# Kernel optimization log

Measured on AMD Instinct MI355X. Metric: run time of the kernel, lower is better.

Reference implementation:

```python
import jax, jax.numpy as jnp
import numpy as np

V = 16384      # total nodes
G = 32         # nodes per graph (512 graphs)
D = 256        # node embedding dim == hidden_size
N = 8          # heads
H = 32         # head size
I = 1024       # intermediate size
LN_EPS = 1e-12


def _layer_norm(x, g, b):
    mu = jnp.mean(x, axis=-1, keepdims=True)
    var = jnp.mean(jnp.square(x - mu), axis=-1, keepdims=True)
    return (x - mu) * jax.lax.rsqrt(var + LN_EPS) * g + b


def setup_inputs() -> dict:
    key = jax.random.key(0)
    ks = jax.random.split(key, 5)
    node_embeddings = jax.random.normal(ks[0], (V, D), jnp.float32)
    # fully-connected pairs within each graph of size G (sorted by source node)
    idx = np.arange(V, dtype=np.int32).reshape(-1, G)          # [num_graphs, G]
    src = np.repeat(idx, G, axis=1).reshape(-1)                # [P]
    dst = np.tile(idx, (1, G)).reshape(-1)                     # [P]
    in_graph_node_pairs = jnp.asarray(np.stack([src, dst], axis=-1))  # [P, 2]
    s = 0.02
    return {
        "node_embeddings": node_embeddings,
        "in_graph_node_pairs": in_graph_node_pairs,
        "W_qkv": jax.random.normal(ks[1], (D, 3 * N * H), jnp.float32) * s,
        "W_o": jax.random.normal(ks[2], (N * H, D), jnp.float32) * s,
        "ln1_g": jnp.ones((D,), jnp.float32),
        "ln1_b": jnp.zeros((D,), jnp.float32),
        "W_i": jax.random.normal(ks[3], (D, I), jnp.float32) * s,
        "W_out2": jax.random.normal(ks[4], (I, D), jnp.float32) * s,
        "ln2_g": jnp.ones((D,), jnp.float32),
        "ln2_b": jnp.zeros((D,), jnp.float32),
    }


def reference(node_embeddings, in_graph_node_pairs, W_qkv, W_o, ln1_g, ln1_b,
              W_i, W_out2, ln2_g, ln2_b):
    nV = node_embeddings.shape[0]
    src = in_graph_node_pairs[:, 0]
    dst = in_graph_node_pairs[:, 1]
    # QKV projection -> [V, N, 3H] -> split
    qkv = (node_embeddings @ W_qkv).reshape(nV, N, 3 * H)
    q, k, v = jnp.split(qkv, 3, axis=-1)                       # each [V, N, H]
    # per-pair scores [P, N]
    scores = jnp.einsum('phi,phi->ph', q[src], k[dst]) / jnp.sqrt(jnp.float32(H))
    # segment softmax over source node, all heads at once
    m = jax.ops.segment_max(scores, src, num_segments=nV)       # [V, N]
    e = jnp.exp(scores - m[src])
    denom = jax.ops.segment_sum(e, src, num_segments=nV)        # [V, N]
    w = e / denom[src]                                          # [P, N]
    # weighted value scatter-sum -> [V, N, H]
    wv = w[:, :, None] * v[dst]
    att = jax.ops.segment_sum(wv, src, num_segments=nV).reshape(nV, N * H)
    # output projection + residual + LN
    pre = _layer_norm(att @ W_o + node_embeddings, ln1_g, ln1_b)
    inter = jax.nn.gelu(pre @ W_i, approximate=False)
    out = _layer_norm(inter @ W_out2 + pre, ln2_g, ln2_b)
    return out
```

## Files before the change

### kernel.cpp

```cpp
#include <hip/hip_runtime.h>
#include <math.h>

#define V 16384
#define D 256
#define NH 256
#define THREE_NH 768
#define IDIM 1024
#define LN_EPS 1e-12f

typedef short s16x8 __attribute__((ext_vector_type(8)));
typedef float f32x4 __attribute__((ext_vector_type(4)));

__device__ inline unsigned short f2bf(float f) {
    unsigned u = __float_as_uint(f);
    u += 0x7fffu + ((u >> 16) & 1u);
    return (unsigned short)(u >> 16);
}
__device__ inline float bf2f(unsigned short s) {
    return __uint_as_float(((unsigned)s) << 16);
}
__device__ inline float bflo(unsigned v) { return __uint_as_float(v << 16); }
__device__ inline float bfhi(unsigned v) { return __uint_as_float(v & 0xffff0000u); }

__device__ inline void gl2lds16(const unsigned short* g, unsigned short* l) {
    __builtin_amdgcn_global_load_lds(
        (__attribute__((address_space(1))) void*)(g),
        (__attribute__((address_space(3))) void*)(l), 16, 0, 0);
}

template <int ROWS_T>
__device__ inline void stage(const unsigned short* __restrict__ src, size_t row0,
                             int ldk, int k0, unsigned short* lds, int wv, int lane) {
    constexpr int PER_WAVE = ROWS_T / 32;
    #pragma unroll
    for (int i = 0; i < PER_WAVE; ++i) {
        const int seg = wv * PER_WAVE + i;
        const int r = seg * 8 + (lane >> 3);
        const int c = (lane & 7) ^ (r & 7);
        gl2lds16(src + (row0 + (size_t)r) * ldk + k0 + c * 8, lds + seg * 512);
    }
}

__device__ inline s16x8 fragld(const unsigned short* lds, int row, int chunk) {
    return *(const s16x8*)&lds[row * 64 + ((chunk ^ (row & 7)) << 3)];
}

__global__ __launch_bounds__(256) void prep(const float* __restrict__ X,
                                            unsigned short* __restrict__ Xb,
                                            const float* __restrict__ Wqkv,
                                            const float* __restrict__ Wo,
                                            const float* __restrict__ Wi,
                                            const float* __restrict__ Wo2,
                                            unsigned short* __restrict__ WqkvT,
                                            unsigned short* __restrict__ WoT,
                                            unsigned short* __restrict__ WiT,
                                            unsigned short* __restrict__ Wo2T) {
    const int b = blockIdx.x, t = threadIdx.x;
    if (b >= 768) {
        int i = (b - 768) * 256 + t;
        float4 v = ((const float4*)X)[i];
        ushort4 o;
        o.x = f2bf(v.x); o.y = f2bf(v.y); o.z = f2bf(v.z); o.w = f2bf(v.w);
        ((ushort4*)Xb)[i] = o;
        return;
    }
    __shared__ float tile[32][33];
    const float* W; unsigned short* Wt; int K, N, bx, by;
    if (b < 192)      { W = Wqkv; Wt = WqkvT; K = 256;  N = 768;  bx = b & 7;          by = b >> 3; }
    else if (b < 256) { W = Wo;   Wt = WoT;   K = 256;  N = 256;  bx = (b - 192) & 7;  by = (b - 192) >> 3; }
    else if (b < 512) { W = Wi;   Wt = WiT;   K = 256;  N = 1024; bx = (b - 256) & 7;  by = (b - 256) >> 3; }
    else              { W = Wo2;  Wt = Wo2T;  K = 1024; N = 256;  bx = (b - 512) & 31; by = (b - 512) >> 5; }
    const int k0 = bx * 32, n0 = by * 32;
    #pragma unroll
    for (int p = 0; p < 4; ++p) {
        int idx = t + p * 256, r = idx >> 5, c = idx & 31;
        tile[r][c] = W[(size_t)(k0 + r) * N + n0 + c];
    }
    __syncthreads();
    #pragma unroll
    for (int p = 0; p < 4; ++p) {
        int idx = t + p * 256, r = idx >> 5, c = idx & 31;
        Wt[(size_t)(n0 + r) * K + k0 + c] = f2bf(tile[c][r]);
    }
}

template <int K, int N, int EPI>
__global__ __launch_bounds__(256) void gemm128(const unsigned short* __restrict__ A,
                                               const unsigned short* __restrict__ Bt,
                                               unsigned short* __restrict__ C) {
    __shared__ unsigned short As[128 * 64];
    __shared__ unsigned short Bs[128 * 64];
    constexpr int NCOL = N / 128;
    const int b = blockIdx.x;
    const int idx = b >> 3;
    const int r0 = ((b & 7) * 16 + idx / NCOL) * 128;
    const int c0 = (idx % NCOL) * 128;
    const int t = threadIdx.x;
    const int wv = t >> 6, lane = t & 63, q = lane >> 4, l16 = lane & 15;
    const int wr = (wv >> 1) * 64, wc = (wv & 1) * 64;
    f32x4 acc[4][4] = {};

    for (int k0 = 0; k0 < K; k0 += 64) {
        __syncthreads();
        stage<128>(A,  (size_t)r0, K, k0, As, wv, lane);
        stage<128>(Bt, (size_t)c0, K, k0, Bs, wv, lane);
        __builtin_amdgcn_s_waitcnt(0);
        __syncthreads();
        #pragma unroll
        for (int kk2 = 0; kk2 < 2; ++kk2) {
            s16x8 af[4], bfr[4];
            #pragma unroll
            for (int mf = 0; mf < 4; ++mf)
                af[mf] = fragld(As, wr + mf * 16 + l16, kk2 * 4 + q);
            #pragma unroll
            for (int nf = 0; nf < 4; ++nf)
                bfr[nf] = fragld(Bs, wc + nf * 16 + l16, kk2 * 4 + q);
            #pragma unroll
            for (int mf = 0; mf < 4; ++mf)
                #pragma unroll
                for (int nf = 0; nf < 4; ++nf)
                    acc[mf][nf] = __builtin_amdgcn_mfma_f32_16x16x32_bf16(af[mf], bfr[nf], acc[mf][nf], 0, 0, 0);
        }
    }

    #pragma unroll
    for (int mf = 0; mf < 4; ++mf)
        #pragma unroll
        for (int nf = 0; nf < 4; ++nf) {
            const int cg = c0 + wc + nf * 16 + l16;
            #pragma unroll
            for (int r = 0; r < 4; ++r) {
                const int rg = r0 + wr + mf * 16 + q * 4 + r;
                float v = acc[mf][nf][r];
                if (EPI == 1) v = 0.5f * v * (1.f + erff(v * 0.70710678118654752f));
                C[(size_t)rg * N + cg] = f2bf(v);
            }
        }
}

template <int K, bool OUTF, bool RESBF>
__global__ __launch_bounds__(256) void gemm_ln(const unsigned short* __restrict__ A,
                                               const unsigned short* __restrict__ Bt,
                                               const void* __restrict__ resv,
                                               const float* __restrict__ gamma,
                                               const float* __restrict__ beta,
                                               float* __restrict__ outf,
                                               unsigned short* __restrict__ outb) {
    __shared__ unsigned short As[2][32 * 64];
    __shared__ unsigned short Bs[2][256 * 64];
    __shared__ float2 partial[4][32];
    __shared__ float2 stats[32];
    const int t = threadIdx.x, r0 = blockIdx.x * 32;
    const int wv = t >> 6, lane = t & 63, q = lane >> 4, l16 = lane & 15;
    const int wc = wv * 64;
    f32x4 acc[2][4] = {};

    for (int k0 = 0; k0 < K; k0 += 128) {
        __syncthreads();
        stage<32>(A, (size_t)r0, K, k0,      As[0], wv, lane);
        stage<32>(A, (size_t)r0, K, k0 + 64, As[1], wv, lane);
        stage<256>(Bt, 0, K, k0,      Bs[0], wv, lane);
        stage<256>(Bt, 0, K, k0 + 64, Bs[1], wv, lane);
        __builtin_amdgcn_s_waitcnt(0);
        __syncthreads();
        #pragma unroll
        for (int sub = 0; sub < 2; ++sub) {
            #pragma unroll
            for (int kk2 = 0; kk2 < 2; ++kk2) {
                s16x8 af[2], bfr[4];
                #pragma unroll
                for (int mf = 0; mf < 2; ++mf)
                    af[mf] = fragld(As[sub], mf * 16 + l16, kk2 * 4 + q);
                #pragma unroll
                for (int nf = 0; nf < 4; ++nf)
                    bfr[nf] = fragld(Bs[sub], wc + nf * 16 + l16, kk2 * 4 + q);
                #pragma unroll
                for (int mf = 0; mf < 2; ++mf)
                    #pragma unroll
                    for (int nf = 0; nf < 4; ++nf)
                        acc[mf][nf] = __builtin_amdgcn_mfma_f32_16x16x32_bf16(af[mf], bfr[nf], acc[mf][nf], 0, 0, 0);
            }
        }
    }

    #pragma unroll
    for (int mf = 0; mf < 2; ++mf)
        #pragma unroll
        for (int nf = 0; nf < 4; ++nf) {
            const int cg = wc + nf * 16 + l16;
            #pragma unroll
            for (int r = 0; r < 4; ++r) {
                const size_t idx = (size_t)(r0 + mf * 16 + q * 4 + r) * NH + cg;
                float rv;
                if (RESBF) rv = bf2f(((const unsigned short*)resv)[idx]);
                else       rv = ((const float*)resv)[idx];
                acc[mf][nf][r] += rv;
            }
        }

    #pragma unroll
    for (int mf = 0; mf < 2; ++mf) {
        float s[4] = {0.f, 0.f, 0.f, 0.f}, ss[4] = {0.f, 0.f, 0.f, 0.f};
        #pragma unroll
        for (int nf = 0; nf < 4; ++nf)
            #pragma unroll
            for (int r = 0; r < 4; ++r) {
                float v = acc[mf][nf][r];
                s[r] += v; ss[r] += v * v;
            }
        #pragma unroll
        for (int off = 1; off < 16; off <<= 1)
            #pragma unroll
            for (int r = 0; r < 4; ++r) {
                s[r]  += __shfl_xor(s[r],  off);
                ss[r] += __shfl_xor(ss[r], off);
            }
        if (l16 == 0)
            #pragma unroll
            for (int r = 0; r < 4; ++r)
                partial[wv][mf * 16 + q * 4 + r] = make_float2(s[r], ss[r]);
    }
    __syncthreads();
    if (t < 32) {
        float s = 0.f, ss = 0.f;
        #pragma unroll
        for (int w = 0; w < 4; ++w) { s += partial[w][t].x; ss += partial[w][t].y; }
        float mu  = s * (1.f / 256.f);
        float var = ss * (1.f / 256.f) - mu * mu;
        stats[t] = make_float2(mu, rsqrtf(var + LN_EPS));
    }
    __syncthreads();

    #pragma unroll
    for (int mf = 0; mf < 2; ++mf)
        #pragma unroll
        for (int nf = 0; nf < 4; ++nf) {
            const int cg = wc + nf * 16 + l16;
            const float g = gamma[cg], b = beta[cg];
            #pragma unroll
            for (int r = 0; r < 4; ++r) {
                const int rl = mf * 16 + q * 4 + r;
                const float2 st = stats[rl];
                float v = (acc[mf][nf][r] - st.x) * st.y * g + b;
                const size_t idx = (size_t)(r0 + rl) * NH + cg;
                if (OUTF) outf[idx] = v;
                else      outb[idx] = f2bf(v);
            }
        }
}

#define LDR 776
__global__ __launch_bounds__(256) void attln(const unsigned short* __restrict__ qkv,
                                             const unsigned short* __restrict__ WoT,
                                             const float* __restrict__ X,
                                             const float* __restrict__ gamma,
                                             const float* __restrict__ beta,
                                             unsigned short* __restrict__ preb) {
    __shared__ unsigned short smem[33536 + 320];
    unsigned short* s  = smem;
    unsigned short* pt = smem + 24832;
    unsigned short* at = smem;
    unsigned short* Bs = smem + 8192;
    float2* partial = (float2*)(smem + 24832);
    float2* stats   = (float2*)(smem + 24832 + 512);

    const int g = blockIdx.x;
    const int t = threadIdx.x;
    const int h = t >> 5, u = t & 31;
    const int ub = u & 7;
    const int us = u >> 3;
    const int qc = h * 96;

    const unsigned short* src = qkv + (size_t)g * 32 * THREE_NH;
    #pragma unroll
    for (int pp = 0; pp < 12; ++pp) {
        int c = t + pp * 256;
        int row = c / 96, col8 = c % 96;
        s16x8 vv = *(const s16x8*)&src[c * 8];
        *(s16x8*)&s[row * LDR + col8 * 8] = vv;
    }
    __syncthreads();

    float sc[4][8];
    #pragma unroll
    for (int di = 0; di < 4; ++di)
        #pragma unroll
        for (int dj = 0; dj < 8; ++dj) sc[di][dj] = 0.f;

    for (int kq = 0; kq < 8; ++kq) {
        float qv[4][4];
        #pragma unroll
        for (int di = 0; di < 4; ++di) {
            uint2 v = *(const uint2*)&s[(ub + 8 * di) * LDR + qc + 4 * kq];
            qv[di][0] = bflo(v.x); qv[di][1] = bfhi(v.x);
            qv[di][2] = bflo(v.y); qv[di][3] = bfhi(v.y);
        }
        #pragma unroll
        for (int dj = 0; dj < 8; ++dj) {
            uint2 v = *(const uint2*)&s[(us + 4 * dj) * LDR + qc + 32 + 4 * kq];
            float kv[4];
            kv[0] = bflo(v.x); kv[1] = bfhi(v.x);
            kv[2] = bflo(v.y); kv[3] = bfhi(v.y);
            #pragma unroll
            for (int di = 0; di < 4; ++di)
                #pragma unroll
                for (int kk = 0; kk < 4; ++kk)
                    sc[di][dj] = fmaf(qv[di][kk], kv[kk], sc[di][dj]);
        }
    }

    #pragma unroll
    for (int di = 0; di < 4; ++di) {
        float m = sc[di][0];
        #pragma unroll
        for (int dj = 1; dj < 8; ++dj) m = fmaxf(m, sc[di][dj]);
        m = fmaxf(m, __shfl_xor(m, 8));
        m = fmaxf(m, __shfl_xor(m, 16));
        float sum = 0.f;
        #pragma unroll
        for (int dj = 0; dj < 8; ++dj) {
            float e = __expf((sc[di][dj] - m) * 0.17677669529663687f);
            sc[di][dj] = e;
            sum += e;
        }
        sum += __shfl_xor(sum, 8);
        sum += __shfl_xor(sum, 16);
        float inv = 1.f / sum;
        const int rb = h * 1088 + (ub + 8 * di) * 34;
        #pragma unroll
        for (int dj = 0; dj < 8; ++dj)
            pt[rb + us + 4 * dj] = f2bf(sc[di][dj] * inv);
    }
    __syncthreads();

    const int vc = qc + 64, d0 = us * 8;
    float o[4][8];
    #pragma unroll
    for (int di = 0; di < 4; ++di)
        #pragma unroll
        for (int dd = 0; dd < 8; ++dd) o[di][dd] = 0.f;

    for (int j = 0; j < 32; ++j) {
        float pv[4];
        #pragma unroll
        for (int di = 0; di < 4; ++di)
            pv[di] = bf2f(pt[h * 1088 + (ub + 8 * di) * 34 + j]);
        #pragma unroll
        for (int dq = 0; dq < 2; ++dq) {
            uint2 v = *(const uint2*)&s[j * LDR + vc + d0 + 4 * dq];
            float v0 = bflo(v.x), v1 = bfhi(v.x), v2 = bflo(v.y), v3 = bfhi(v.y);
            #pragma unroll
            for (int di = 0; di < 4; ++di) {
                o[di][dq * 4 + 0] = fmaf(pv[di], v0, o[di][dq * 4 + 0]);
                o[di][dq * 4 + 1] = fmaf(pv[di], v1, o[di][dq * 4 + 1]);
                o[di][dq * 4 + 2] = fmaf(pv[di], v2, o[di][dq * 4 + 2]);
                o[di][dq * 4 + 3] = fmaf(pv[di], v3, o[di][dq * 4 + 3]);
            }
        }
    }
    __syncthreads();

    {
        const int col = h * 32 + d0;
        const int kb = col >> 6, c = (col & 63) >> 3;
        #pragma unroll
        for (int di = 0; di < 4; ++di) {
            const int i = ub + 8 * di;
            s16x8 ov;
            #pragma unroll
            for (int dd = 0; dd < 8; ++dd) ov[dd] = (short)f2bf(o[di][dd]);
            *(s16x8*)&at[kb * 2048 + i * 64 + ((c ^ (i & 7)) << 3)] = ov;
        }
    }

    const int wv = t >> 6, lane = t & 63, q = lane >> 4, l16 = lane & 15;
    const int wc = wv * 64;
    const int r0 = g * 32;
    f32x4 acc[2][4] = {};

    for (int k0 = 0; k0 < 256; k0 += 64) {
        __syncthreads();
        stage<256>(WoT, 0, 256, k0, Bs, wv, lane);
        __builtin_amdgcn_s_waitcnt(0);
        __syncthreads();
        const unsigned short* atk = at + (k0 >> 6) * 2048;
        #pragma unroll
        for (int kk2 = 0; kk2 < 2; ++kk2) {
            s16x8 af[2], bfr[4];
            #pragma unroll
            for (int mf = 0; mf < 2; ++mf)
                af[mf] = fragld(atk, mf * 16 + l16, kk2 * 4 + q);
            #pragma unroll
            for (int nf = 0; nf < 4; ++nf)
                bfr[nf] = fragld(Bs, wc + nf * 16 + l16, kk2 * 4 + q);
            #pragma unroll
            for (int mf = 0; mf < 2; ++mf)
                #pragma unroll
                for (int nf = 0; nf < 4; ++nf)
                    acc[mf][nf] = __builtin_amdgcn_mfma_f32_16x16x32_bf16(af[mf], bfr[nf], acc[mf][nf], 0, 0, 0);
        }
    }

    #pragma unroll
    for (int mf = 0; mf < 2; ++mf)
        #pragma unroll
        for (int nf = 0; nf < 4; ++nf) {
            const int cg = wc + nf * 16 + l16;
            #pragma unroll
            for (int r = 0; r < 4; ++r)
                acc[mf][nf][r] += X[(size_t)(r0 + mf * 16 + q * 4 + r) * NH + cg];
        }

    #pragma unroll
    for (int mf = 0; mf < 2; ++mf) {
        float sp[4] = {0.f, 0.f, 0.f, 0.f}, ssp[4] = {0.f, 0.f, 0.f, 0.f};
        #pragma unroll
        for (int nf = 0; nf < 4; ++nf)
            #pragma unroll
            for (int r = 0; r < 4; ++r) {
                float v = acc[mf][nf][r];
                sp[r] += v; ssp[r] += v * v;
            }
        #pragma unroll
        for (int off = 1; off < 16; off <<= 1)
            #pragma unroll
            for (int r = 0; r < 4; ++r) {
                sp[r]  += __shfl_xor(sp[r],  off);
                ssp[r] += __shfl_xor(ssp[r], off);
            }
        if (l16 == 0)
            #pragma unroll
            for (int r = 0; r < 4; ++r)
                partial[wv * 32 + mf * 16 + q * 4 + r] = make_float2(sp[r], ssp[r]);
    }
    __syncthreads();
    if (t < 32) {
        float sv = 0.f, ssv = 0.f;
        #pragma unroll
        for (int w = 0; w < 4; ++w) { sv += partial[w * 32 + t].x; ssv += partial[w * 32 + t].y; }
        float mu  = sv * (1.f / 256.f);
        float var = ssv * (1.f / 256.f) - mu * mu;
        stats[t] = make_float2(mu, rsqrtf(var + LN_EPS));
    }
    __syncthreads();

    #pragma unroll
    for (int mf = 0; mf < 2; ++mf)
        #pragma unroll
        for (int nf = 0; nf < 4; ++nf) {
            const int cg = wc + nf * 16 + l16;
            const float gm = gamma[cg], bt = beta[cg];
            #pragma unroll
            for (int r = 0; r < 4; ++r) {
                const int rl = mf * 16 + q * 4 + r;
                const float2 st = stats[rl];
                float v = (acc[mf][nf][r] - st.x) * st.y * gm + bt;
                preb[(size_t)(r0 + rl) * NH + cg] = f2bf(v);
            }
        }
}

extern "C" void kernel_launch(void* const* d_in, const int* in_sizes, int n_in,
                              void* d_out, int out_size, void* d_ws, size_t ws_size,
                              hipStream_t stream) {
    const float* X      = (const float*)d_in[0];
    const float* W_qkv  = (const float*)d_in[2];
    const float* W_o    = (const float*)d_in[3];
    const float* ln1_g  = (const float*)d_in[4];
    const float* ln1_b  = (const float*)d_in[5];
    const float* W_i    = (const float*)d_in[6];
    const float* W_out2 = (const float*)d_in[7];
    const float* ln2_g  = (const float*)d_in[8];
    const float* ln2_b  = (const float*)d_in[9];
    float* out = (float*)d_out;

    char* ws = (char*)d_ws;
    unsigned short* Xbf   = (unsigned short*)(ws);
    unsigned short* qkvb  = (unsigned short*)(ws + 8388608);
    unsigned short* preb  = (unsigned short*)(ws + 58720256);
    unsigned short* WqkvT = (unsigned short*)(ws + 67108864);
    unsigned short* WoT   = (unsigned short*)(ws + 67502080);
    unsigned short* WiT   = (unsigned short*)(ws + 67633152);
    unsigned short* Wo2T  = (unsigned short*)(ws + 68157440);
    unsigned short* interb = (unsigned short*)(ws);

    dim3 blk(256);
    hipLaunchKernelGGL(prep, dim3(768 + V * D / 4 / 256), blk, 0, stream,
                       X, Xbf, W_qkv, W_o, W_i, W_out2, WqkvT, WoT, WiT, Wo2T);

    hipLaunchKernelGGL((gemm128<D, THREE_NH, 0>), dim3(V / 128 * (THREE_NH / 128)), blk, 0, stream,
                       Xbf, WqkvT, qkvb);
    hipLaunchKernelGGL(attln, dim3(V / 32), blk, 0, stream,
                       qkvb, WoT, X, ln1_g, ln1_b, preb);
    hipLaunchKernelGGL((gemm128<D, IDIM, 1>), dim3(V / 128 * (IDIM / 128)), blk, 0, stream,
                       preb, WiT, interb);
    hipLaunchKernelGGL((gemm_ln<IDIM, true, true>), dim3(V / 32), blk, 0, stream,
                       interb, Wo2T, (const void*)preb, ln2_g, ln2_b, out, (unsigned short*)nullptr);
}
```

Measured before the change: 158.5 us.

## Load GEMM fragments directly from global memory, drop LDS staging, use fast erf

All GEMM kernels (QKV, intermediate, output+LN, and the Wo projection inside the attention kernel) now load MFMA operand fragments straight from global memory into registers. This removes the LDS staging through global_load_lds and its per-k-step barriers. The GELU epilogue also replaces erff with a polynomial erf approximation using __expf. The cost is redundant global/L2 traffic, since waves no longer share tiles through LDS and the 16-byte row-strided loads are poorly coalesced. The erf approximation (about 1e-7 error) also slightly changes numerics.

```diff
diff --git a/kernel.cpp b/kernel.cpp
--- a/kernel.cpp
+++ b/kernel.cpp
@@ -22,23 +22,13 @@
 __device__ inline float bflo(unsigned v) { return __uint_as_float(v << 16); }
 __device__ inline float bfhi(unsigned v) { return __uint_as_float(v & 0xffff0000u); }
 
-__device__ inline void gl2lds16(const unsigned short* g, unsigned short* l) {
-    __builtin_amdgcn_global_load_lds(
-        (__attribute__((address_space(1))) void*)(g),
-        (__attribute__((address_space(3))) void*)(l), 16, 0, 0);
-}
-
-template <int ROWS_T>
-__device__ inline void stage(const unsigned short* __restrict__ src, size_t row0,
-                             int ldk, int k0, unsigned short* lds, int wv, int lane) {
-    constexpr int PER_WAVE = ROWS_T / 32;
-    #pragma unroll
-    for (int i = 0; i < PER_WAVE; ++i) {
-        const int seg = wv * PER_WAVE + i;
-        const int r = seg * 8 + (lane >> 3);
-        const int c = (lane & 7) ^ (r & 7);
-        gl2lds16(src + (row0 + (size_t)r) * ldk + k0 + c * 8, lds + seg * 512);
-    }
+__device__ inline float fast_erf(float x) {
+    float ax = fabsf(x);
+    float t  = 1.f / fmaf(0.3275911f, ax, 1.f);
+    float p  = fmaf(fmaf(fmaf(fmaf(1.061405429f, t, -1.453152027f), t,
+                              1.421413741f), t, -0.284496736f), t, 0.254829592f);
+    float e  = 1.f - p * t * __expf(-ax * ax);
+    return copysignf(e, x);
 }
 
 __device__ inline s16x8 fragld(const unsigned short* lds, int row, int chunk) {
@@ -85,11 +75,9 @@
 }
 
 template <int K, int N, int EPI>
-__global__ __launch_bounds__(256) void gemm128(const unsigned short* __restrict__ A,
-                                               const unsigned short* __restrict__ Bt,
-                                               unsigned short* __restrict__ C) {
-    __shared__ unsigned short As[128 * 64];
-    __shared__ unsigned short Bs[128 * 64];
+__global__ __launch_bounds__(256) void gemm_direct(const unsigned short* __restrict__ A,
+                                                   const unsigned short* __restrict__ Bt,
+                                                   unsigned short* __restrict__ C) {
     constexpr int NCOL = N / 128;
     const int b = blockIdx.x;
     const int idx = b >> 3;
@@ -100,27 +88,29 @@
     const int wr = (wv >> 1) * 64, wc = (wv & 1) * 64;
     f32x4 acc[4][4] = {};
 
+    const unsigned short* Ap = A  + (size_t)(r0 + wr + l16) * K;
+    const unsigned short* Bp = Bt + (size_t)(c0 + wc + l16) * K;
+
+    #pragma unroll
     for (int k0 = 0; k0 < K; k0 += 64) {
-        __syncthreads();
-        stage<128>(A,  (size_t)r0, K, k0, As, wv, lane);
-        stage<128>(Bt, (size_t)c0, K, k0, Bs, wv, lane);
-        __builtin_amdgcn_s_waitcnt(0);
-        __syncthreads();
-        #pragma unroll
-        for (int kk2 = 0; kk2 < 2; ++kk2) {
-            s16x8 af[4], bfr[4];
-            #pragma unroll
-            for (int mf = 0; mf < 4; ++mf)
-                af[mf] = fragld(As, wr + mf * 16 + l16, kk2 * 4 + q);
-            #pragma unroll
-            for (int nf = 0; nf < 4; ++nf)
-                bfr[nf] = fragld(Bs, wc + nf * 16 + l16, kk2 * 4 + q);
+        s16x8 af[4][2], bfr[4][2];
+        #pragma unroll
+        for (int mf = 0; mf < 4; ++mf)
+            #pragma unroll
+            for (int kk2 = 0; kk2 < 2; ++kk2)
+                af[mf][kk2] = *(const s16x8*)&Ap[(size_t)mf * 16 * K + k0 + (kk2 * 4 + q) * 8];
+        #pragma unroll
+        for (int nf = 0; nf < 4; ++nf)
+            #pragma unroll
+            for (int kk2 = 0; kk2 < 2; ++kk2)
+                bfr[nf][kk2] = *(const s16x8*)&Bp[(size_t)nf * 16 * K + k0 + (kk2 * 4 + q) * 8];
+        #pragma unroll
+        for (int kk2 = 0; kk2 < 2; ++kk2)
             #pragma unroll
             for (int mf = 0; mf < 4; ++mf)
                 #pragma unroll
                 for (int nf = 0; nf < 4; ++nf)
-                    acc[mf][nf] = __builtin_amdgcn_mfma_f32_16x16x32_bf16(af[mf], bfr[nf], acc[mf][nf], 0, 0, 0);
-        }
+                    acc[mf][nf] = __builtin_amdgcn_mfma_f32_16x16x32_bf16(af[mf][kk2], bfr[nf][kk2], acc[mf][nf], 0, 0, 0);
     }
 
     #pragma unroll
@@ -132,22 +122,20 @@
             for (int r = 0; r < 4; ++r) {
                 const int rg = r0 + wr + mf * 16 + q * 4 + r;
                 float v = acc[mf][nf][r];
-                if (EPI == 1) v = 0.5f * v * (1.f + erff(v * 0.70710678118654752f));
+                if (EPI == 1) v = 0.5f * v * (1.f + fast_erf(v * 0.70710678118654752f));
                 C[(size_t)rg * N + cg] = f2bf(v);
             }
         }
 }
 
 template <int K, bool OUTF, bool RESBF>
-__global__ __launch_bounds__(256) void gemm_ln(const unsigned short* __restrict__ A,
-                                               const unsigned short* __restrict__ Bt,
-                                               const void* __restrict__ resv,
-                                               const float* __restrict__ gamma,
-                                               const float* __restrict__ beta,
-                                               float* __restrict__ outf,
-                                               unsigned short* __restrict__ outb) {
-    __shared__ unsigned short As[2][32 * 64];
-    __shared__ unsigned short Bs[2][256 * 64];
+__global__ __launch_bounds__(256) void gemm_ln_direct(const unsigned short* __restrict__ A,
+                                                      const unsigned short* __restrict__ Bt,
+                                                      const void* __restrict__ resv,
+                                                      const float* __restrict__ gamma,
+                                                      const float* __restrict__ beta,
+                                                      float* __restrict__ outf,
+                                                      unsigned short* __restrict__ outb) {
     __shared__ float2 partial[4][32];
     __shared__ float2 stats[32];
     const int t = threadIdx.x, r0 = blockIdx.x * 32;
@@ -155,32 +143,29 @@
     const int wc = wv * 64;
     f32x4 acc[2][4] = {};
 
-    for (int k0 = 0; k0 < K; k0 += 128) {
-        __syncthreads();
-        stage<32>(A, (size_t)r0, K, k0,      As[0], wv, lane);
-        stage<32>(A, (size_t)r0, K, k0 + 64, As[1], wv, lane);
-        stage<256>(Bt, 0, K, k0,      Bs[0], wv, lane);
-        stage<256>(Bt, 0, K, k0 + 64, Bs[1], wv, lane);
-        __builtin_amdgcn_s_waitcnt(0);
-        __syncthreads();
-        #pragma unroll
-        for (int sub = 0; sub < 2; ++sub) {
-            #pragma unroll
-            for (int kk2 = 0; kk2 < 2; ++kk2) {
-                s16x8 af[2], bfr[4];
-                #pragma unroll
-                for (int mf = 0; mf < 2; ++mf)
-                    af[mf] = fragld(As[sub], mf * 16 + l16, kk2 * 4 + q);
+    const unsigned short* Ap = A  + (size_t)(r0 + l16) * K;
+    const unsigned short* Bp = Bt + (size_t)(wc + l16) * K;
+
+    #pragma unroll
+    for (int k0 = 0; k0 < K; k0 += 64) {
+        s16x8 af[2][2], bfr[4][2];
+        #pragma unroll
+        for (int mf = 0; mf < 2; ++mf)
+            #pragma unroll
+            for (int kk2 = 0; kk2 < 2; ++kk2)
+                af[mf][kk2] = *(const s16x8*)&Ap[(size_t)mf * 16 * K + k0 + (kk2 * 4 + q) * 8];
+        #pragma unroll
+        for (int nf = 0; nf < 4; ++nf)
+            #pragma unroll
+            for (int kk2 = 0; kk2 < 2; ++kk2)
+                bfr[nf][kk2] = *(const s16x8*)&Bp[(size_t)nf * 16 * K + k0 + (kk2 * 4 + q) * 8];
+        #pragma unroll
+        for (int kk2 = 0; kk2 < 2; ++kk2)
+            #pragma unroll
+            for (int mf = 0; mf < 2; ++mf)
                 #pragma unroll
                 for (int nf = 0; nf < 4; ++nf)
-                    bfr[nf] = fragld(Bs[sub], wc + nf * 16 + l16, kk2 * 4 + q);
-                #pragma unroll
-                for (int mf = 0; mf < 2; ++mf)
-                    #pragma unroll
-                    for (int nf = 0; nf < 4; ++nf)
-                        acc[mf][nf] = __builtin_amdgcn_mfma_f32_16x16x32_bf16(af[mf], bfr[nf], acc[mf][nf], 0, 0, 0);
-            }
-        }
+                    acc[mf][nf] = __builtin_amdgcn_mfma_f32_16x16x32_bf16(af[mf][kk2], bfr[nf][kk2], acc[mf][nf], 0, 0, 0);
     }
 
     #pragma unroll
@@ -260,7 +245,6 @@
     unsigned short* s  = smem;
     unsigned short* pt = smem + 24832;
     unsigned short* at = smem;
-    unsigned short* Bs = smem + 8192;
     float2* partial = (float2*)(smem + 24832);
     float2* stats   = (float2*)(smem + 24832 + 512);
 
@@ -372,18 +356,18 @@
             *(s16x8*)&at[kb * 2048 + i * 64 + ((c ^ (i & 7)) << 3)] = ov;
         }
     }
+    __syncthreads();
 
     const int wv = t >> 6, lane = t & 63, q = lane >> 4, l16 = lane & 15;
     const int wc = wv * 64;
     const int r0 = g * 32;
     f32x4 acc[2][4] = {};
 
-    for (int k0 = 0; k0 < 256; k0 += 64) {
-        __syncthreads();
-        stage<256>(WoT, 0, 256, k0, Bs, wv, lane);
-        __builtin_amdgcn_s_waitcnt(0);
-        __syncthreads();
-        const unsigned short* atk = at + (k0 >> 6) * 2048;
+    const unsigned short* Bp = WoT + (size_t)(wc + l16) * NH;
+
+    #pragma unroll
+    for (int kc = 0; kc < 4; ++kc) {
+        const unsigned short* atk = at + kc * 2048;
         #pragma unroll
         for (int kk2 = 0; kk2 < 2; ++kk2) {
             s16x8 af[2], bfr[4];
@@ -392,7 +376,7 @@
                 af[mf] = fragld(atk, mf * 16 + l16, kk2 * 4 + q);
             #pragma unroll
             for (int nf = 0; nf < 4; ++nf)
-                bfr[nf] = fragld(Bs, wc + nf * 16 + l16, kk2 * 4 + q);
+                bfr[nf] = *(const s16x8*)&Bp[(size_t)nf * 16 * NH + kc * 64 + (kk2 * 4 + q) * 8];
             #pragma unroll
             for (int mf = 0; mf < 2; ++mf)
                 #pragma unroll
@@ -488,12 +472,12 @@
     hipLaunchKernelGGL(prep, dim3(768 + V * D / 4 / 256), blk, 0, stream,
                        X, Xbf, W_qkv, W_o, W_i, W_out2, WqkvT, WoT, WiT, Wo2T);
 
-    hipLaunchKernelGGL((gemm128<D, THREE_NH, 0>), dim3(V / 128 * (THREE_NH / 128)), blk, 0, stream,
+    hipLaunchKernelGGL((gemm_direct<D, THREE_NH, 0>), dim3(V / 128 * (THREE_NH / 128)), blk, 0, stream,
                        Xbf, WqkvT, qkvb);
     hipLaunchKernelGGL(attln, dim3(V / 32), blk, 0, stream,
                        qkvb, WoT, X, ln1_g, ln1_b, preb);
-    hipLaunchKernelGGL((gemm128<D, IDIM, 1>), dim3(V / 128 * (IDIM / 128)), blk, 0, stream,
+    hipLaunchKernelGGL((gemm_direct<D, IDIM, 1>), dim3(V / 128 * (IDIM / 128)), blk, 0, stream,
                        preb, WiT, interb);
-    hipLaunchKernelGGL((gemm_ln<IDIM, true, true>), dim3(V / 32), blk, 0, stream,
+    hipLaunchKernelGGL((gemm_ln_direct<IDIM, true, true>), dim3(V / 32), blk, 0, stream,
                        interb, Wo2T, (const void*)preb, ln2_g, ln2_b, out, (unsigned short*)nullptr);
 }
```

Result: slower. 224.5 us (+41.7%).

## Double-buffer LDS staging in all GEMM kernels and use a polynomial erf for GELU

Applied to the files above, without the earlier changes.

Converts the K loops of gemm128, gemm_ln and the attention output projection to double-buffered LDS staging. The next K tile is loaded asynchronously while MFMAs run on the current one, so there is one barrier per step instead of two and global latency is hidden. The Wo stage is issued before the attention output is written to LDS, and shared memory grows to hold the extra buffers. The GELU epilogue also swaps erff for an Abramowitz-Stegun polynomial (about 1e-7 error), which is cheaper but slightly less accurate.

```diff
diff --git a/kernel.cpp b/kernel.cpp
--- a/kernel.cpp
+++ b/kernel.cpp
@@ -21,6 +21,15 @@
 }
 __device__ inline float bflo(unsigned v) { return __uint_as_float(v << 16); }
 __device__ inline float bfhi(unsigned v) { return __uint_as_float(v & 0xffff0000u); }
+
+__device__ inline float fast_erf(float x) {
+    float ax = fabsf(x);
+    float t  = 1.f / fmaf(0.3275911f, ax, 1.f);
+    float p  = fmaf(fmaf(fmaf(fmaf(1.061405429f, t, -1.453152027f), t,
+                              1.421413741f), t, -0.284496736f), t, 0.254829592f);
+    float e  = 1.f - p * t * __expf(-ax * ax);
+    return copysignf(e, x);
+}
 
 __device__ inline void gl2lds16(const unsigned short* g, unsigned short* l) {
     __builtin_amdgcn_global_load_lds(
@@ -88,9 +97,10 @@
 __global__ __launch_bounds__(256) void gemm128(const unsigned short* __restrict__ A,
                                                const unsigned short* __restrict__ Bt,
                                                unsigned short* __restrict__ C) {
-    __shared__ unsigned short As[128 * 64];
-    __shared__ unsigned short Bs[128 * 64];
+    __shared__ unsigned short As[2][128 * 64];
+    __shared__ unsigned short Bs[2][128 * 64];
     constexpr int NCOL = N / 128;
+    constexpr int NT = K / 64;
     const int b = blockIdx.x;
     const int idx = b >> 3;
     const int r0 = ((b & 7) * 16 + idx / NCOL) * 128;
@@ -100,27 +110,35 @@
     const int wr = (wv >> 1) * 64, wc = (wv & 1) * 64;
     f32x4 acc[4][4] = {};
 
-    for (int k0 = 0; k0 < K; k0 += 64) {
-        __syncthreads();
-        stage<128>(A,  (size_t)r0, K, k0, As, wv, lane);
-        stage<128>(Bt, (size_t)c0, K, k0, Bs, wv, lane);
-        __builtin_amdgcn_s_waitcnt(0);
-        __syncthreads();
+    stage<128>(A,  (size_t)r0, K, 0, As[0], wv, lane);
+    stage<128>(Bt, (size_t)c0, K, 0, Bs[0], wv, lane);
+    __builtin_amdgcn_s_waitcnt(0);
+    __syncthreads();
+
+    #pragma unroll
+    for (int kt = 0; kt < NT; ++kt) {
+        const int cur = kt & 1;
+        if (kt + 1 < NT) {
+            stage<128>(A,  (size_t)r0, K, (kt + 1) * 64, As[cur ^ 1], wv, lane);
+            stage<128>(Bt, (size_t)c0, K, (kt + 1) * 64, Bs[cur ^ 1], wv, lane);
+        }
         #pragma unroll
         for (int kk2 = 0; kk2 < 2; ++kk2) {
             s16x8 af[4], bfr[4];
             #pragma unroll
             for (int mf = 0; mf < 4; ++mf)
-                af[mf] = fragld(As, wr + mf * 16 + l16, kk2 * 4 + q);
+                af[mf] = fragld(As[cur], wr + mf * 16 + l16, kk2 * 4 + q);
             #pragma unroll
             for (int nf = 0; nf < 4; ++nf)
-                bfr[nf] = fragld(Bs, wc + nf * 16 + l16, kk2 * 4 + q);
+                bfr[nf] = fragld(Bs[cur], wc + nf * 16 + l16, kk2 * 4 + q);
             #pragma unroll
             for (int mf = 0; mf < 4; ++mf)
                 #pragma unroll
                 for (int nf = 0; nf < 4; ++nf)
                     acc[mf][nf] = __builtin_amdgcn_mfma_f32_16x16x32_bf16(af[mf], bfr[nf], acc[mf][nf], 0, 0, 0);
         }
+        __builtin_amdgcn_s_waitcnt(0);
+        __syncthreads();
     }
 
     #pragma unroll
@@ -132,7 +150,7 @@
             for (int r = 0; r < 4; ++r) {
                 const int rg = r0 + wr + mf * 16 + q * 4 + r;
                 float v = acc[mf][nf][r];
-                if (EPI == 1) v = 0.5f * v * (1.f + erff(v * 0.70710678118654752f));
+                if (EPI == 1) v = 0.5f * v * (1.f + fast_erf(v * 0.70710678118654752f));
                 C[(size_t)rg * N + cg] = f2bf(v);
             }
         }
@@ -150,37 +168,41 @@
     __shared__ unsigned short Bs[2][256 * 64];
     __shared__ float2 partial[4][32];
     __shared__ float2 stats[32];
+    constexpr int NT = K / 64;
     const int t = threadIdx.x, r0 = blockIdx.x * 32;
     const int wv = t >> 6, lane = t & 63, q = lane >> 4, l16 = lane & 15;
     const int wc = wv * 64;
     f32x4 acc[2][4] = {};
 
-    for (int k0 = 0; k0 < K; k0 += 128) {
-        __syncthreads();
-        stage<32>(A, (size_t)r0, K, k0,      As[0], wv, lane);
-        stage<32>(A, (size_t)r0, K, k0 + 64, As[1], wv, lane);
-        stage<256>(Bt, 0, K, k0,      Bs[0], wv, lane);
-        stage<256>(Bt, 0, K, k0 + 64, Bs[1], wv, lane);
+    stage<32>(A, (size_t)r0, K, 0, As[0], wv, lane);
+    stage<256>(Bt, 0, K, 0, Bs[0], wv, lane);
+    __builtin_amdgcn_s_waitcnt(0);
+    __syncthreads();
+
+    #pragma unroll
+    for (int kt = 0; kt < NT; ++kt) {
+        const int cur = kt & 1;
+        if (kt + 1 < NT) {
+            stage<32>(A, (size_t)r0, K, (kt + 1) * 64, As[cur ^ 1], wv, lane);
+            stage<256>(Bt, 0, K, (kt + 1) * 64, Bs[cur ^ 1], wv, lane);
+        }
+        #pragma unroll
+        for (int kk2 = 0; kk2 < 2; ++kk2) {
+            s16x8 af[2], bfr[4];
+            #pragma unroll
+            for (int mf = 0; mf < 2; ++mf)
+                af[mf] = fragld(As[cur], mf * 16 + l16, kk2 * 4 + q);
+            #pragma unroll
+            for (int nf = 0; nf < 4; ++nf)
+                bfr[nf] = fragld(Bs[cur], wc + nf * 16 + l16, kk2 * 4 + q);
+            #pragma unroll
+            for (int mf = 0; mf < 2; ++mf)
+                #pragma unroll
+                for (int nf = 0; nf < 4; ++nf)
+                    acc[mf][nf] = __builtin_amdgcn_mfma_f32_16x16x32_bf16(af[mf], bfr[nf], acc[mf][nf], 0, 0, 0);
+        }
         __builtin_amdgcn_s_waitcnt(0);
         __syncthreads();
-        #pragma unroll
-        for (int sub = 0; sub < 2; ++sub) {
-            #pragma unroll
-            for (int kk2 = 0; kk2 < 2; ++kk2) {
-                s16x8 af[2], bfr[4];
-                #pragma unroll
-                for (int mf = 0; mf < 2; ++mf)
-                    af[mf] = fragld(As[sub], mf * 16 + l16, kk2 * 4 + q);
-                #pragma unroll
-                for (int nf = 0; nf < 4; ++nf)
-                    bfr[nf] = fragld(Bs[sub], wc + nf * 16 + l16, kk2 * 4 + q);
-                #pragma unroll
-                for (int mf = 0; mf < 2; ++mf)
-                    #pragma unroll
-                    for (int nf = 0; nf < 4; ++nf)
-                        acc[mf][nf] = __builtin_amdgcn_mfma_f32_16x16x32_bf16(af[mf], bfr[nf], acc[mf][nf], 0, 0, 0);
-            }
-        }
     }
 
     #pragma unroll
@@ -256,13 +278,14 @@
                                              const float* __restrict__ gamma,
                                              const float* __restrict__ beta,
                                              unsigned short* __restrict__ preb) {
-    __shared__ unsigned short smem[33536 + 320];
+    __shared__ unsigned short smem[40960];
     unsigned short* s  = smem;
     unsigned short* pt = smem + 24832;
     unsigned short* at = smem;
-    unsigned short* Bs = smem + 8192;
-    float2* partial = (float2*)(smem + 24832);
-    float2* stats   = (float2*)(smem + 24832 + 512);
+    unsigned short* Bs0 = smem + 8192;
+    unsigned short* Bs1 = smem + 24576;
+    float2* partial = (float2*)(smem + 8192);
+    float2* stats   = (float2*)(smem + 8192 + 512);
 
     const int g = blockIdx.x;
     const int t = threadIdx.x;
@@ -360,6 +383,8 @@
     }
     __syncthreads();
 
+    const int wv = t >> 6, lane = t & 63, q = lane >> 4, l16 = lane & 15;
+    stage<256>(WoT, 0, 256, 0, Bs0, wv, lane);
     {
         const int col = h * 32 + d0;
         const int kb = col >> 6, c = (col & 63) >> 3;
@@ -372,18 +397,21 @@
             *(s16x8*)&at[kb * 2048 + i * 64 + ((c ^ (i & 7)) << 3)] = ov;
         }
     }
-
-    const int wv = t >> 6, lane = t & 63, q = lane >> 4, l16 = lane & 15;
+    __builtin_amdgcn_s_waitcnt(0);
+    __syncthreads();
+
     const int wc = wv * 64;
     const int r0 = g * 32;
     f32x4 acc[2][4] = {};
 
-    for (int k0 = 0; k0 < 256; k0 += 64) {
-        __syncthreads();
-        stage<256>(WoT, 0, 256, k0, Bs, wv, lane);
-        __builtin_amdgcn_s_waitcnt(0);
-        __syncthreads();
-        const unsigned short* atk = at + (k0 >> 6) * 2048;
+    #pragma unroll
+    for (int kc = 0; kc < 4; ++kc) {
+        unsigned short* Bcur = (kc & 1) ? Bs1 : Bs0;
+        if (kc + 1 < 4) {
+            unsigned short* Bnxt = (kc & 1) ? Bs0 : Bs1;
+            stage<256>(WoT, 0, 256, (kc + 1) * 64, Bnxt, wv, lane);
+        }
+        const unsigned short* atk = at + kc * 2048;
         #pragma unroll
         for (int kk2 = 0; kk2 < 2; ++kk2) {
             s16x8 af[2], bfr[4];
@@ -392,13 +420,15 @@
                 af[mf] = fragld(atk, mf * 16 + l16, kk2 * 4 + q);
             #pragma unroll
             for (int nf = 0; nf < 4; ++nf)
-                bfr[nf] = fragld(Bs, wc + nf * 16 + l16, kk2 * 4 + q);
+                bfr[nf] = fragld(Bcur, wc + nf * 16 + l16, kk2 * 4 + q);
             #pragma unroll
             for (int mf = 0; mf < 2; ++mf)
                 #pragma unroll
                 for (int nf = 0; nf < 4; ++nf)
                     acc[mf][nf] = __builtin_amdgcn_mfma_f32_16x16x32_bf16(af[mf], bfr[nf], acc[mf][nf], 0, 0, 0);
         }
+        __builtin_amdgcn_s_waitcnt(0);
+        __syncthreads();
     }
 
     #pragma unroll
```

Result: slower. 169.2 us (+6.8%).

## Compute per-graph attention with MFMA and use polynomial erf in GELU

Applied to the files above, without the earlier changes.

Replaces the scalar FMA QK^T and PV loops in the fused attention+LN kernel with bf16 MFMA 16x16x32 instructions. K is staged via direct global-to-LDS loads, V is transposed into swizzled LDS, and softmax normalization is deferred to the output. Also swaps erff in the GELU epilogue for an Abramowitz-Stegun polynomial approximation. The aim is to cut VALU and LDS work in attention and in the GELU epilogue, at the cost of slightly different rounding (unnormalized bf16 probabilities) and an approximate erf.

```diff
diff --git a/kernel.cpp b/kernel.cpp
--- a/kernel.cpp
+++ b/kernel.cpp
@@ -7,6 +7,7 @@
 #define THREE_NH 768
 #define IDIM 1024
 #define LN_EPS 1e-12f
+#define SCL 0.17677669529663687f
 
 typedef short s16x8 __attribute__((ext_vector_type(8)));
 typedef float f32x4 __attribute__((ext_vector_type(4)));
@@ -19,8 +20,15 @@
 __device__ inline float bf2f(unsigned short s) {
     return __uint_as_float(((unsigned)s) << 16);
 }
-__device__ inline float bflo(unsigned v) { return __uint_as_float(v << 16); }
-__device__ inline float bfhi(unsigned v) { return __uint_as_float(v & 0xffff0000u); }
+
+__device__ inline float fast_erf(float x) {
+    float ax = fabsf(x);
+    float t  = 1.f / fmaf(0.3275911f, ax, 1.f);
+    float p  = fmaf(fmaf(fmaf(fmaf(1.061405429f, t, -1.453152027f), t,
+                              1.421413741f), t, -0.284496736f), t, 0.254829592f);
+    float e  = 1.f - p * t * __expf(-ax * ax);
+    return copysignf(e, x);
+}
 
 __device__ inline void gl2lds16(const unsigned short* g, unsigned short* l) {
     __builtin_amdgcn_global_load_lds(
@@ -132,7 +140,7 @@
             for (int r = 0; r < 4; ++r) {
                 const int rg = r0 + wr + mf * 16 + q * 4 + r;
                 float v = acc[mf][nf][r];
-                if (EPI == 1) v = 0.5f * v * (1.f + erff(v * 0.70710678118654752f));
+                if (EPI == 1) v = 0.5f * v * (1.f + fast_erf(v * 0.70710678118654752f));
                 C[(size_t)rg * N + cg] = f2bf(v);
             }
         }
@@ -249,131 +257,140 @@
         }
 }
 
-#define LDR 776
 __global__ __launch_bounds__(256) void attln(const unsigned short* __restrict__ qkv,
                                              const unsigned short* __restrict__ WoT,
                                              const float* __restrict__ X,
                                              const float* __restrict__ gamma,
                                              const float* __restrict__ beta,
                                              unsigned short* __restrict__ preb) {
-    __shared__ unsigned short smem[33536 + 320];
-    unsigned short* s  = smem;
-    unsigned short* pt = smem + 24832;
+    __shared__ unsigned short smem[25216];
+    unsigned short* Ks = smem;
+    unsigned short* Vt = smem + 8192;
+    unsigned short* Ps = smem + 16384;
     unsigned short* at = smem;
     unsigned short* Bs = smem + 8192;
-    float2* partial = (float2*)(smem + 24832);
-    float2* stats   = (float2*)(smem + 24832 + 512);
-
-    const int g = blockIdx.x;
-    const int t = threadIdx.x;
-    const int h = t >> 5, u = t & 31;
-    const int ub = u & 7;
-    const int us = u >> 3;
-    const int qc = h * 96;
-
+    float2* partial = (float2*)(smem + 24576);
+    float2* stats   = (float2*)(smem + 24576 + 512);
+
+    const int g = blockIdx.x, t = threadIdx.x;
+    const int wv = t >> 6, lane = t & 63, q = lane >> 4, l16 = lane & 15;
     const unsigned short* src = qkv + (size_t)g * 32 * THREE_NH;
-    #pragma unroll
-    for (int pp = 0; pp < 12; ++pp) {
-        int c = t + pp * 256;
-        int row = c / 96, col8 = c % 96;
-        s16x8 vv = *(const s16x8*)&src[c * 8];
-        *(s16x8*)&s[row * LDR + col8 * 8] = vv;
-    }
-    __syncthreads();
-
-    float sc[4][8];
-    #pragma unroll
-    for (int di = 0; di < 4; ++di)
-        #pragma unroll
-        for (int dj = 0; dj < 8; ++dj) sc[di][dj] = 0.f;
-
-    for (int kq = 0; kq < 8; ++kq) {
-        float qv[4][4];
-        #pragma unroll
-        for (int di = 0; di < 4; ++di) {
-            uint2 v = *(const uint2*)&s[(ub + 8 * di) * LDR + qc + 4 * kq];
-            qv[di][0] = bflo(v.x); qv[di][1] = bfhi(v.x);
-            qv[di][2] = bflo(v.y); qv[di][3] = bfhi(v.y);
-        }
-        #pragma unroll
-        for (int dj = 0; dj < 8; ++dj) {
-            uint2 v = *(const uint2*)&s[(us + 4 * dj) * LDR + qc + 32 + 4 * kq];
-            float kv[4];
-            kv[0] = bflo(v.x); kv[1] = bfhi(v.x);
-            kv[2] = bflo(v.y); kv[3] = bfhi(v.y);
-            #pragma unroll
-            for (int di = 0; di < 4; ++di)
+
+    s16x8 qf[2][2];
+    #pragma unroll
+    for (int hh = 0; hh < 2; ++hh)
+        #pragma unroll
+        for (int mf = 0; mf < 2; ++mf)
+            qf[hh][mf] = *(const s16x8*)&src[(size_t)(mf * 16 + l16) * THREE_NH +
+                                             (wv * 2 + hh) * 96 + q * 8];
+
+    s16x8 vld[4];
+    int vh[4], vj[4], vdc[4];
+    #pragma unroll
+    for (int i = 0; i < 4; ++i) {
+        int cid = i * 256 + t;
+        vh[i] = cid >> 7; int rem = cid & 127; vj[i] = rem >> 2; vdc[i] = rem & 3;
+        vld[i] = *(const s16x8*)&src[(size_t)vj[i] * THREE_NH + vh[i] * 96 + 64 + vdc[i] * 8];
+    }
+
+    #pragma unroll
+    for (int i = 0; i < 4; ++i) {
+        int ck = (wv * 4 + i) * 64 + lane;
+        int h = ck >> 7, j = (ck >> 2) & 31, c = ck & 3;
+        gl2lds16(src + (size_t)j * THREE_NH + h * 96 + 32 + c * 8, Ks + (wv * 4 + i) * 512);
+    }
+
+    #pragma unroll
+    for (int i = 0; i < 4; ++i)
+        #pragma unroll
+        for (int e = 0; e < 8; ++e) {
+            int d = vdc[i] * 8 + e;
+            Vt[vh[i] * 1024 + d * 32 + ((((vj[i] >> 3) ^ ((d >> 2) & 3))) << 3) + (vj[i] & 7)] =
+                (unsigned short)vld[i][e];
+        }
+
+    __builtin_amdgcn_s_waitcnt(0);
+    __syncthreads();
+
+    f32x4 sacc[2][2][2] = {};
+    #pragma unroll
+    for (int hh = 0; hh < 2; ++hh) {
+        const int h = wv * 2 + hh;
+        #pragma unroll
+        for (int nf = 0; nf < 2; ++nf) {
+            s16x8 kf = *(const s16x8*)&Ks[h * 1024 + (nf * 16 + l16) * 32 + q * 8];
+            #pragma unroll
+            for (int mf = 0; mf < 2; ++mf)
+                sacc[hh][mf][nf] = __builtin_amdgcn_mfma_f32_16x16x32_bf16(
+                    qf[hh][mf], kf, sacc[hh][mf][nf], 0, 0, 0);
+        }
+    }
+
+    float inv[2][2][4];
+    #pragma unroll
+    for (int hh = 0; hh < 2; ++hh) {
+        const int h = wv * 2 + hh;
+        #pragma unroll
+        for (int mf = 0; mf < 2; ++mf)
+            #pragma unroll
+            for (int r = 0; r < 4; ++r) {
+                float a0 = sacc[hh][mf][0][r], a1 = sacc[hh][mf][1][r];
+                float m = fmaxf(a0, a1);
+                m = fmaxf(m, __shfl_xor(m, 1));
+                m = fmaxf(m, __shfl_xor(m, 2));
+                m = fmaxf(m, __shfl_xor(m, 4));
+                m = fmaxf(m, __shfl_xor(m, 8));
+                float e0 = __expf((a0 - m) * SCL);
+                float e1 = __expf((a1 - m) * SCL);
+                float sm = e0 + e1;
+                sm += __shfl_xor(sm, 1);
+                sm += __shfl_xor(sm, 2);
+                sm += __shfl_xor(sm, 4);
+                sm += __shfl_xor(sm, 8);
+                inv[hh][mf][r] = 1.f / sm;
+                const int row = mf * 16 + q * 4 + r;
+                const int base = h * 1024 + row * 32 + (l16 & 7);
+                Ps[base + ((((l16 >> 3) ^ q)) << 3)]       = f2bf(e0);
+                Ps[base + ((((2 + (l16 >> 3)) ^ q)) << 3)] = f2bf(e1);
+            }
+    }
+
+    f32x4 oacc[2][2][2] = {};
+    #pragma unroll
+    for (int hh = 0; hh < 2; ++hh) {
+        const int h = wv * 2 + hh;
+        const int sw = (l16 >> 2) & 3;
+        s16x8 pa[2], vb[2];
+        #pragma unroll
+        for (int mf = 0; mf < 2; ++mf)
+            pa[mf] = *(const s16x8*)&Ps[h * 1024 + (mf * 16 + l16) * 32 + ((q ^ sw) << 3)];
+        #pragma unroll
+        for (int nf = 0; nf < 2; ++nf)
+            vb[nf] = *(const s16x8*)&Vt[h * 1024 + (nf * 16 + l16) * 32 + ((q ^ sw) << 3)];
+        #pragma unroll
+        for (int mf = 0; mf < 2; ++mf)
+            #pragma unroll
+            for (int nf = 0; nf < 2; ++nf)
+                oacc[hh][mf][nf] = __builtin_amdgcn_mfma_f32_16x16x32_bf16(
+                    pa[mf], vb[nf], oacc[hh][mf][nf], 0, 0, 0);
+    }
+    __syncthreads();
+
+    #pragma unroll
+    for (int hh = 0; hh < 2; ++hh)
+        #pragma unroll
+        for (int mf = 0; mf < 2; ++mf)
+            #pragma unroll
+            for (int nf = 0; nf < 2; ++nf)
                 #pragma unroll
-                for (int kk = 0; kk < 4; ++kk)
-                    sc[di][dj] = fmaf(qv[di][kk], kv[kk], sc[di][dj]);
-        }
-    }
-
-    #pragma unroll
-    for (int di = 0; di < 4; ++di) {
-        float m = sc[di][0];
-        #pragma unroll
-        for (int dj = 1; dj < 8; ++dj) m = fmaxf(m, sc[di][dj]);
-        m = fmaxf(m, __shfl_xor(m, 8));
-        m = fmaxf(m, __shfl_xor(m, 16));
-        float sum = 0.f;
-        #pragma unroll
-        for (int dj = 0; dj < 8; ++dj) {
-            float e = __expf((sc[di][dj] - m) * 0.17677669529663687f);
-            sc[di][dj] = e;
-            sum += e;
-        }
-        sum += __shfl_xor(sum, 8);
-        sum += __shfl_xor(sum, 16);
-        float inv = 1.f / sum;
-        const int rb = h * 1088 + (ub + 8 * di) * 34;
-        #pragma unroll
-        for (int dj = 0; dj < 8; ++dj)
-            pt[rb + us + 4 * dj] = f2bf(sc[di][dj] * inv);
-    }
-    __syncthreads();
-
-    const int vc = qc + 64, d0 = us * 8;
-    float o[4][8];
-    #pragma unroll
-    for (int di = 0; di < 4; ++di)
-        #pragma unroll
-        for (int dd = 0; dd < 8; ++dd) o[di][dd] = 0.f;
-
-    for (int j = 0; j < 32; ++j) {
-        float pv[4];
-        #pragma unroll
-        for (int di = 0; di < 4; ++di)
-            pv[di] = bf2f(pt[h * 1088 + (ub + 8 * di) * 34 + j]);
-        #pragma unroll
-        for (int dq = 0; dq < 2; ++dq) {
-            uint2 v = *(const uint2*)&s[j * LDR + vc + d0 + 4 * dq];
-            float v0 = bflo(v.x), v1 = bfhi(v.x), v2 = bflo(v.y), v3 = bfhi(v.y);
-            #pragma unroll
-            for (int di = 0; di < 4; ++di) {
-                o[di][dq * 4 + 0] = fmaf(pv[di], v0, o[di][dq * 4 + 0]);
-                o[di][dq * 4 + 1] = fmaf(pv[di], v1, o[di][dq * 4 + 1]);
-                o[di][dq * 4 + 2] = fmaf(pv[di], v2, o[di][dq * 4 + 2]);
-                o[di][dq * 4 + 3] = fmaf(pv[di], v3, o[di][dq * 4 + 3]);
-            }
-        }
-    }
-    __syncthreads();
-
-    {
-        const int col = h * 32 + d0;
-        const int kb = col >> 6, c = (col & 63) >> 3;
-        #pragma unroll
-        for (int di = 0; di < 4; ++di) {
-            const int i = ub + 8 * di;
-            s16x8 ov;
-            #pragma unroll
-            for (int dd = 0; dd < 8; ++dd) ov[dd] = (short)f2bf(o[di][dd]);
-            *(s16x8*)&at[kb * 2048 + i * 64 + ((c ^ (i & 7)) << 3)] = ov;
-        }
-    }
-
-    const int wv = t >> 6, lane = t & 63, q = lane >> 4, l16 = lane & 15;
+                for (int r = 0; r < 4; ++r) {
+                    float val = oacc[hh][mf][nf][r] * inv[hh][mf][r];
+                    const int i = mf * 16 + q * 4 + r;
+                    const int col = (wv * 2 + hh) * 32 + nf * 16 + l16;
+                    const int kb = col >> 6, c = (col >> 3) & 7;
+                    at[kb * 2048 + i * 64 + ((c ^ (i & 7)) << 3) + (col & 7)] = f2bf(val);
+                }
+
     const int wc = wv * 64;
     const int r0 = g * 32;
     f32x4 acc[2][4] = {};
```

Result: no change. 160.3 us (+1.2%).
